# Performance work log

Hardware: AMD Instinct MI355X
Metric: run time of the kernel (lower is better)

Reference implementation:

```python
import jax, jax.numpy as jnp
import numpy as np

B, T, N, DIN, H, E, K, HM, CH, HOR, DOUT = 64, 12, 307, 1, 64, 10, 2, 16, 14, 12, 1
EPS = 1e-12


def setup_inputs() -> dict:
    key = jax.random.key(0)
    ks = jax.random.split(key, 16)
    rn = lambda k, s, sc=0.1: jax.random.normal(k, s, dtype=jnp.float32) * sc
    return {
        "hyper_source": jax.random.normal(ks[0], (B, CH, T, N), dtype=jnp.float32),
        "source": jax.random.normal(ks[1], (B, T, N, DIN), dtype=jnp.float32),
        "adj": jax.random.uniform(ks[2], (N, N), dtype=jnp.float32),
        "node_embeddings": rn(ks[3], (N, E), 1.0),
        "main_weights_pool": rn(ks[4], (E, H, DIN)),
        "hyper_W": rn(ks[5], (CH, H)),
        "hyper_b": jnp.zeros((H,), jnp.float32),
        "mask_W1": rn(ks[6], (H, HM)),
        "mask_W2": rn(ks[7], (HM, E)),
        "gate_Wpool": rn(ks[8], (E, K, 2 * DIN + H, 2 * H)),
        "gate_bpool": rn(ks[9], (E, 2 * H)),
        "upd_Wpool": rn(ks[10], (E, K, 2 * DIN + H, H)),
        "upd_bpool": rn(ks[11], (E, H)),
        "ln_gamma": jnp.ones((H,), jnp.float32),
        "ln_beta": jnp.zeros((H,), jnp.float32),
        "end_W": rn(ks[12], (HOR * DOUT, H)),
        "end_b": jnp.zeros((HOR * DOUT,), jnp.float32),
    }


def _forward(hyper_source, source, adj, node_embeddings, main_weights_pool,
             hyper_W, hyper_b, mask_W1, mask_W2, gate_Wpool, gate_bpool,
             upd_Wpool, upd_bpool, ln_gamma, ln_beta, end_W, end_b):
    # HyperNet: chunked long-history signal -> per-node per-step hidden h [B,N,T,H]
    h = jnp.tanh(jnp.einsum('bctn,ch->bnth', hyper_source, hyper_W) + hyper_b)
    # adaptive input channel: einsum('bnld,ndi->blni') with per-node weights
    weights_h = jnp.einsum('nd,dhi->nhi', node_embeddings, main_weights_pool)  # [N,H,DIN]
    x_adapt = jnp.einsum('bnlh,nhi->blni', h, weights_h)                       # [B,T,N,DIN]
    x = jnp.concatenate([x_adapt, source], axis=-1)                            # [B,T,N,2*DIN]
    # static Chebyshev supports (cheb_k=2): identity + mix(normalized adj, adaptive graph)
    adj_n = adj / jnp.clip(adj.sum(-1, keepdims=True), 1e-6)
    adapt = jax.nn.softmax(jax.nn.relu(node_embeddings @ node_embeddings.T), axis=1)
    A = 0.5 * (adj_n + adapt)
    supports = jnp.stack([jnp.eye(N, dtype=x.dtype), A])                       # [K,N,N]
    # per-node graph-conv weights generated from node embeddings
    gate_W = jnp.einsum('nd,dkio->nkio', node_embeddings, gate_Wpool)
    gate_b = node_embeddings @ gate_bpool
    upd_W = jnp.einsum('nd,dkio->nkio', node_embeddings, upd_Wpool)
    upd_b = node_embeddings @ upd_bpool

    def gconv(sup_b, xin, Wn, bn):
        xg = jnp.einsum('bknm,bmi->bnki', sup_b, xin)
        return jnp.einsum('bnki,nkio->bno', xg, Wn) + bn

    def step(state, inp):
        xt, ht = inp  # [B,N,2*DIN], [B,N,H]
        # dynamic graph sparsification mask from hypernet state
        logits = jnp.einsum('bne,me->bnm', (ht @ mask_W1) @ mask_W2, node_embeddings)
        mask = jax.nn.sigmoid(logits)                # [B,N,N]
        sup_b = supports[None] * mask[:, None]       # [B,K,N,N]
        xs = jnp.concatenate([xt, state], axis=-1)
        zr = jax.nn.sigmoid(gconv(sup_b, xs, gate_W, gate_b))
        z, r = jnp.split(zr, 2, axis=-1)
        cand = jnp.concatenate([xt, z * state], axis=-1)
        hc = jnp.tanh(gconv(sup_b, cand, upd_W, upd_b))
        return r * state + (1.0 - r) * hc, None

    init = jnp.zeros((x.shape[0], N, H), x.dtype)
    state, _ = jax.lax.scan(step, init,
                            (jnp.swapaxes(x, 0, 1), jnp.transpose(h, (2, 0, 1, 3))))
    # layernorm(eps=1e-12); dropout is identity at eval
    mu = state.mean(-1, keepdims=True)
    var = ((state - mu) ** 2).mean(-1, keepdims=True)
    xn = (state - mu) / jnp.sqrt(var + EPS) * ln_gamma + ln_beta
    # end_conv: Conv2d(1, HOR*DOUT, kernel=(1,H)) == per-node linear H -> HOR*DOUT
    out = jnp.einsum('bnh,oh->bon', xn, end_W) + end_b[None, :, None]
    out = out.reshape(-1, HOR, DOUT, N).transpose(0, 1, 3, 2)  # [B,HOR,N,DOUT]
    return out


def reference(hyper_source, source, adj, node_embeddings, main_weights_pool,
              hyper_W, hyper_b, mask_W1, mask_W2, gate_Wpool, gate_bpool,
              upd_Wpool, upd_bpool, ln_gamma, ln_beta, end_W, end_b):
    return _forward(hyper_source, source, adj, node_embeddings, main_weights_pool,
                    hyper_W, hyper_b, mask_W1, mask_W2, gate_Wpool, gate_bpool,
                    upd_Wpool, upd_bpool, ln_gamma, ln_beta, end_W, end_b)
```

## Files before the change

### kernel.cpp

```cpp
#include <hip/hip_runtime.h>
#include <hip/hip_bf16.h>

#define N_ 307
#define B_ 64
#define T_ 12
#define H_ 64
#define E_ 10
#define CH_ 14
#define HM_ 16
#define I2_ 66
#define GO_ 128
#define UO_ 64
#define QG_ (2 * I2_ * GO_)
#define QU_ (2 * I2_ * UO_)
#define TBN_ (T_ * B_ * N_)
#define WMP_ 320

__device__ __forceinline__ float wsum(float v) {
    #pragma unroll
    for (int off = 32; off; off >>= 1) v += __shfl_xor(v, off);
    return v;
}
__device__ __forceinline__ float wmax(float v) {
    #pragma unroll
    for (int off = 32; off; off >>= 1) v = fmaxf(v, __shfl_xor(v, off));
    return v;
}
__device__ __forceinline__ float sigm(float x) { return 1.f / (1.f + __expf(-x)); }
__device__ __forceinline__ float ftanh(float x) { return 1.f - 2.f / (__expf(2.f * x) + 1.f); }
__device__ __forceinline__ float bcast(float v, int l) {
    return __int_as_float(__builtin_amdgcn_readlane(__float_as_int(v), l));
}
__device__ __forceinline__ unsigned short f2bf(float f) {
    unsigned u = __float_as_uint(f);
    u += 0x7FFFu + ((u >> 16) & 1u);
    return (unsigned short)(u >> 16);
}
__device__ __forceinline__ float bf2f(unsigned short s) {
    return __uint_as_float((unsigned)s << 16);
}

__global__ void A_kernel(const float* __restrict__ adj, const float* __restrict__ nemb,
                         float* __restrict__ A) {
    const int n = blockIdx.x;
    const int lane = threadIdx.x;
    float en[E_];
    #pragma unroll
    for (int d = 0; d < E_; ++d) en[d] = nemb[n * E_ + d];
    float asum = 0.f;
    for (int m = lane; m < N_; m += 64) asum += adj[n * N_ + m];
    asum = fmaxf(wsum(asum), 1e-6f);
    float g[5]; bool valid[5];
    float mx = -1e30f;
    #pragma unroll
    for (int it = 0; it < 5; ++it) {
        int m = lane + it * 64;
        valid[it] = (m < N_);
        float dt = 0.f;
        if (valid[it]) {
            #pragma unroll
            for (int e = 0; e < E_; ++e) dt += en[e] * nemb[m * E_ + e];
            dt = fmaxf(dt, 0.f);
            mx = fmaxf(mx, dt);
        }
        g[it] = dt;
    }
    mx = wmax(mx);
    float se = 0.f;
    #pragma unroll
    for (int it = 0; it < 5; ++it)
        if (valid[it]) { g[it] = __expf(g[it] - mx); se += g[it]; }
    se = wsum(se);
    float inv = 1.f / se;
    #pragma unroll
    for (int it = 0; it < 5; ++it) {
        int m = lane + it * 64;
        if (valid[it]) A[n * N_ + m] = 0.5f * (adj[n * N_ + m] / asum + g[it] * inv);
    }
}

__device__ __forceinline__ float embdot(const float* __restrict__ nemb, int n,
                                        const float* __restrict__ pool, int Q, int q) {
    float a = 0.f;
    #pragma unroll
    for (int d = 0; d < E_; ++d) a += nemb[n * E_ + d] * pool[d * Q + q];
    return a;
}

__global__ __launch_bounds__(256) void gen_kernel(
    const float* __restrict__ nemb,
    const float* __restrict__ gWp, const float* __restrict__ gbp,
    const float* __restrict__ uWp, const float* __restrict__ ubp,
    const float* __restrict__ mwp,
    const float* __restrict__ W1, const float* __restrict__ W2,
    float* __restrict__ gW, float* __restrict__ gb,
    float* __restrict__ uW, float* __restrict__ ub,
    float* __restrict__ wh_t, float* __restrict__ W12) {
    const int e0 = N_ * QG_;
    const int e1 = e0 + N_ * GO_;
    const int e2 = e1 + N_ * QU_;
    const int e3 = e2 + N_ * UO_;
    const int e4 = e3 + N_ * H_;
    const int e5 = e4 + H_ * E_;
    int idx = blockIdx.x * 256 + threadIdx.x;
    if (idx < e0) {
        int n = idx / QG_, q = idx % QG_;
        gW[idx] = embdot(nemb, n, gWp, QG_, q);
    } else if (idx < e1) {
        int i = idx - e0; int n = i / GO_, q = i % GO_;
        gb[i] = embdot(nemb, n, gbp, GO_, q);
    } else if (idx < e2) {
        int i = idx - e1; int n = i / QU_, q = i % QU_;
        uW[i] = embdot(nemb, n, uWp, QU_, q);
    } else if (idx < e3) {
        int i = idx - e2; int n = i / UO_, q = i % UO_;
        ub[i] = embdot(nemb, n, ubp, UO_, q);
    } else if (idx < e4) {
        int i = idx - e3; int n = i / H_, q = i % H_;
        wh_t[q * N_ + n] = embdot(nemb, n, mwp, H_, q);
    } else if (idx < e5) {
        int i = idx - e4; int j = i / E_, e = i % E_;
        float a = 0.f;
        #pragma unroll
        for (int q = 0; q < HM_; ++q) a += W1[j * HM_ + q] * W2[q * E_ + e];
        W12[i] = a;
    }
}

__global__ __launch_bounds__(256) void hyper2_kernel(
    const float* __restrict__ hs, const float* __restrict__ src,
    const float* __restrict__ hyper_W, const float* __restrict__ hyper_b,
    const float* __restrict__ wh_t, const float* __restrict__ W12,
    float* __restrict__ x0, float* __restrict__ x1, float* __restrict__ emb) {
    const int tb = blockIdx.y;
    const int t = tb / B_, b = tb % B_;
    const int n = blockIdx.x * 256 + threadIdx.x;
    const bool act = (n < N_);
    const int nc = act ? n : N_ - 1;
    float hsv[CH_];
    #pragma unroll
    for (int c = 0; c < CH_; ++c)
        hsv[c] = hs[((b * CH_ + c) * T_ + t) * N_ + nc];
    float ax0 = 0.f;
    float ae[E_] = {};
    #pragma unroll 8
    for (int j = 0; j < H_; ++j) {
        float hj = hyper_b[j];
        #pragma unroll
        for (int c = 0; c < CH_; ++c) hj = fmaf(hsv[c], hyper_W[c * H_ + j], hj);
        hj = ftanh(hj);
        ax0 = fmaf(hj, wh_t[j * N_ + nc], ax0);
        #pragma unroll
        for (int e = 0; e < E_; ++e) ae[e] = fmaf(hj, W12[j * E_ + e], ae[e]);
    }
    if (act) {
        const int tbn = tb * N_ + n;
        x0[tbn] = ax0;
        x1[tbn] = src[(b * T_ + t) * N_ + n];
        #pragma unroll
        for (int e = 0; e < E_; ++e) emb[e * TBN_ + tbn] = ae[e];
    }
}

__global__ __launch_bounds__(256) void wm_kernel(
    const float* __restrict__ A, const float* __restrict__ emb,
    const float* __restrict__ nemb, const float* __restrict__ x0,
    const float* __restrict__ x1, unsigned short* __restrict__ Wm,
    float* __restrict__ dmask, float* __restrict__ aggx, int t) {
    const int wid = __builtin_amdgcn_readfirstlane(blockIdx.x * 4 + (threadIdx.x >> 6));
    const int lane = threadIdx.x & 63;
    const int b = wid / N_;
    const int n = wid % N_;
    const int tbn = (t * B_ + b) * N_ + n;
    const int xb = tbn - n;
    float et[E_];
    #pragma unroll
    for (int d = 0; d < E_; ++d) et[d] = emb[(size_t)d * TBN_ + tbn];
    unsigned short* wr = Wm + (size_t)(b * N_ + n) * WMP_;
    float a0 = 0.f, a1 = 0.f;
    #pragma unroll
    for (int c = 0; c < 5; ++c) {
        int m = c * 64 + lane;
        bool v = (m < N_);
        int mc = v ? m : 0;
        float dt = 0.f;
        #pragma unroll
        for (int d = 0; d < E_; ++d) dt += et[d] * nemb[mc * E_ + d];
        float sg = sigm(dt);
        float w = v ? A[n * N_ + mc] * sg : 0.f;
        wr[m] = v ? f2bf(w) : (unsigned short)0;
        if (v) {
            if (m == n) dmask[tbn] = sg;
            a0 += w * x0[xb + mc];
            a1 += w * x1[xb + mc];
        }
    }
    a0 = wsum(a0);
    a1 = wsum(a1);
    if (lane == 0) {
        aggx[(size_t)tbn * 2] = a0;
        aggx[(size_t)tbn * 2 + 1] = a1;
    }
}

__global__ __launch_bounds__(512) void aggS_kernel(
    const unsigned short* __restrict__ Wm, const float* __restrict__ Sin,
    float* __restrict__ aggS) {
    __shared__ float s_lds[128 * 64];
    const int tid = threadIdx.x;
    const int lane = tid & 63;
    const int wv = tid >> 6;
    const int b = blockIdx.y;
    const int nb = blockIdx.x * 32 + wv * 4;
    int roff[4];
    #pragma unroll
    for (int r = 0; r < 4; ++r) {
        int nr = nb + r; if (nr > N_ - 1) nr = N_ - 1;
        roff[r] = __builtin_amdgcn_readfirstlane((b * N_ + nr) * WMP_);
    }
    float acc[4] = {0.f, 0.f, 0.f, 0.f};
    const float4* s4 = (const float4*)(Sin + (size_t)b * N_ * 64);
    float4* d4 = (float4*)s_lds;
    #pragma unroll
    for (int sck = 0; sck < 3; ++sck) {
        const int mbase = sck * 128;
        const int nrows = (sck < 2) ? 128 : 64;
        if (sck) __syncthreads();
        for (int idx = tid; idx < nrows * 16; idx += 512) {
            int row = mbase + (idx >> 4);
            int rc = (row < N_) ? row : N_ - 1;
            d4[idx] = s4[rc * 16 + (idx & 15)];
        }
        __syncthreads();
        for (int sub = 0; sub < nrows; sub += 64) {
            const int m0 = mbase + sub;
            float wf0 = bf2f(Wm[roff[0] + m0 + lane]);
            float wf1 = bf2f(Wm[roff[1] + m0 + lane]);
            float wf2 = bf2f(Wm[roff[2] + m0 + lane]);
            float wf3 = bf2f(Wm[roff[3] + m0 + lane]);
            #pragma unroll 8
            for (int mm = 0; mm < 64; ++mm) {
                float sv = s_lds[(sub + mm) * 64 + lane];
                acc[0] = fmaf(bcast(wf0, mm), sv, acc[0]);
                acc[1] = fmaf(bcast(wf1, mm), sv, acc[1]);
                acc[2] = fmaf(bcast(wf2, mm), sv, acc[2]);
                acc[3] = fmaf(bcast(wf3, mm), sv, acc[3]);
            }
        }
    }
    #pragma unroll
    for (int r = 0; r < 4; ++r) {
        int nr = nb + r;
        if (nr < N_) aggS[((size_t)b * N_ + nr) * 64 + lane] = acc[r];
    }
}

__global__ __launch_bounds__(256) void gate_mm_kernel(
    const float* __restrict__ gate_W, const float* __restrict__ gate_b,
    const float* __restrict__ x0, const float* __restrict__ x1,
    const float* __restrict__ S, const float* __restrict__ dmask,
    const float* __restrict__ aggx, const float* __restrict__ aggS,
    float* __restrict__ zs, float* __restrict__ rbuf, int t) {
    __shared__ float W_s[132][64];
    __shared__ float xg_s[64][132];
    const int oh = blockIdx.x, n = blockIdx.y;
    const int tid = threadIdx.x;
    for (int idx = tid; idx < 132 * 64; idx += 256) {
        int row = idx >> 6, op = idx & 63;
        int col = (op < 32) ? (oh * 32 + op) : (64 + oh * 32 + (op - 32));
        W_s[row][op] = gate_W[(n * 132 + row) * GO_ + col];
    }
    for (int idx = tid; idx < 64 * 132; idx += 256) {
        int b = idx / 132, i = idx % 132;
        int tb = (t * B_ + b) * N_ + n;
        float v;
        if (i < 66) {
            float xs = (i == 0) ? x0[tb] : (i == 1) ? x1[tb] : S[(b * N_ + n) * 64 + (i - 2)];
            v = dmask[tb] * xs;
        } else {
            int i2 = i - 66;
            v = (i2 < 2) ? aggx[(size_t)tb * 2 + i2] : aggS[(b * N_ + n) * 64 + (i2 - 2)];
        }
        xg_s[b][i] = v;
    }
    __syncthreads();
    const int bl = (tid >> 3) * 2, og = tid & 7;
    float acc[2][8] = {};
    for (int i = 0; i < 132; ++i) {
        float xv0 = xg_s[bl][i], xv1 = xg_s[bl + 1][i];
        #pragma unroll
        for (int r = 0; r < 8; ++r) {
            float wv = W_s[i][og * 8 + r];
            acc[0][r] = fmaf(xv0, wv, acc[0][r]);
            acc[1][r] = fmaf(xv1, wv, acc[1][r]);
        }
    }
    __syncthreads();
    float* zr_s = &xg_s[0][0];
    #pragma unroll
    for (int q = 0; q < 2; ++q) {
        #pragma unroll
        for (int r = 0; r < 8; ++r) {
            int op = og * 8 + r;
            int col = (op < 32) ? (oh * 32 + op) : (64 + oh * 32 + (op - 32));
            zr_s[(bl + q) * 64 + op] = sigm(acc[q][r] + gate_b[n * GO_ + col]);
        }
    }
    __syncthreads();
    for (int idx = tid; idx < 64 * 32; idx += 256) {
        int b = idx >> 5, jl = idx & 31;
        int j = oh * 32 + jl;
        float z = zr_s[b * 64 + jl];
        float rr = zr_s[b * 64 + 32 + jl];
        int sidx = (b * N_ + n) * 64 + j;
        zs[sidx] = z * S[sidx];
        rbuf[sidx] = rr;
    }
}

__global__ __launch_bounds__(256) void upd_mm_kernel(
    const float* __restrict__ upd_W, const float* __restrict__ upd_b,
    const float* __restrict__ x0, const float* __restrict__ x1,
    const float* __restrict__ zsrc, const float* __restrict__ dmask,
    const float* __restrict__ aggx, const float* __restrict__ aggS,
    const float* __restrict__ rbuf, float* __restrict__ S, int t) {
    __shared__ float W_s[132][64];
    __shared__ float xg_s[64][132];
    const int n = blockIdx.x;
    const int tid = threadIdx.x;
    for (int idx = tid; idx < 132 * 64; idx += 256) {
        int row = idx >> 6, op = idx & 63;
        W_s[row][op] = upd_W[(n * 132 + row) * UO_ + op];
    }
    for (int idx = tid; idx < 64 * 132; idx += 256) {
        int b = idx / 132, i = idx % 132;
        int tb = (t * B_ + b) * N_ + n;
        float v;
        if (i < 66) {
            float xs = (i == 0) ? x0[tb] : (i == 1) ? x1[tb] : zsrc[(b * N_ + n) * 64 + (i - 2)];
            v = dmask[tb] * xs;
        } else {
            int i2 = i - 66;
            v = (i2 < 2) ? aggx[(size_t)tb * 2 + i2] : aggS[(b * N_ + n) * 64 + (i2 - 2)];
        }
        xg_s[b][i] = v;
    }
    __syncthreads();
    const int bl = (tid >> 3) * 2, og = tid & 7;
    float acc[2][8] = {};
    for (int i = 0; i < 132; ++i) {
        float xv0 = xg_s[bl][i], xv1 = xg_s[bl + 1][i];
        #pragma unroll
        for (int r = 0; r < 8; ++r) {
            float wv = W_s[i][og * 8 + r];
            acc[0][r] = fmaf(xv0, wv, acc[0][r]);
            acc[1][r] = fmaf(xv1, wv, acc[1][r]);
        }
    }
    #pragma unroll
    for (int q = 0; q < 2; ++q) {
        int b = bl + q;
        #pragma unroll
        for (int r = 0; r < 8; ++r) {
            int op = og * 8 + r;
            float hc = ftanh(acc[q][r] + upd_b[n * UO_ + op]);
            int sidx = (b * N_ + n) * 64 + op;
            float rr = rbuf[sidx];
            float sv = S[sidx];
            S[sidx] = rr * sv + (1.f - rr) * hc;
        }
    }
}

__global__ __launch_bounds__(256) void final_kernel(
    const float* __restrict__ S, const float* __restrict__ gamma,
    const float* __restrict__ beta, const float* __restrict__ endW,
    const float* __restrict__ endb, float* __restrict__ out) {
    const int wid = blockIdx.x * 4 + (threadIdx.x >> 6);
    const int lane = threadIdx.x & 63;
    const int b = wid / N_, n = wid % N_;
    float s = S[wid * 64 + lane];
    float mu = wsum(s) * (1.f / 64.f);
    float d = s - mu;
    float var = wsum(d * d) * (1.f / 64.f);
    float xn = d / sqrtf(var + 1e-12f) * gamma[lane] + beta[lane];
    #pragma unroll
    for (int o = 0; o < 12; ++o) {
        float dot = wsum(xn * endW[o * 64 + lane]);
        if (lane == o) out[(b * 12 + o) * N_ + n] = dot + endb[o];
    }
}

extern "C" void kernel_launch(void* const* d_in, const int* in_sizes, int n_in,
                              void* d_out, int out_size, void* d_ws, size_t ws_size,
                              hipStream_t stream) {
    const float* hyper_source = (const float*)d_in[0];
    const float* source       = (const float*)d_in[1];
    const float* adj          = (const float*)d_in[2];
    const float* nemb         = (const float*)d_in[3];
    const float* mwpool       = (const float*)d_in[4];
    const float* hyper_W      = (const float*)d_in[5];
    const float* hyper_b      = (const float*)d_in[6];
    const float* mask_W1      = (const float*)d_in[7];
    const float* mask_W2      = (const float*)d_in[8];
    const float* gate_Wpool   = (const float*)d_in[9];
    const float* gate_bpool   = (const float*)d_in[10];
    const float* upd_Wpool    = (const float*)d_in[11];
    const float* upd_bpool    = (const float*)d_in[12];
    const float* ln_gamma     = (const float*)d_in[13];
    const float* ln_beta      = (const float*)d_in[14];
    const float* end_W        = (const float*)d_in[15];
    const float* end_b        = (const float*)d_in[16];
    float* out = (float*)d_out;

    float* ws = (float*)d_ws;
    size_t off = 0;
    auto alloc = [&](size_t nf) {
        float* p = ws + off;
        off += (nf + 255) & ~(size_t)255;
        return p;
    };
    float* A      = alloc((size_t)N_ * N_);
    float* wh_t   = alloc((size_t)N_ * H_);
    float* W12    = alloc((size_t)H_ * E_);
    float* gate_W = alloc((size_t)N_ * QG_);
    float* gate_b = alloc((size_t)N_ * GO_);
    float* upd_W  = alloc((size_t)N_ * QU_);
    float* upd_b  = alloc((size_t)N_ * UO_);
    float* x0     = alloc((size_t)TBN_);
    float* x1     = alloc((size_t)TBN_);
    float* emb    = alloc((size_t)TBN_ * E_);
    float* dmask  = alloc((size_t)TBN_);
    float* aggx   = alloc((size_t)TBN_ * 2);
    float* S      = alloc((size_t)B_ * N_ * H_);
    float* zs     = alloc((size_t)B_ * N_ * H_);
    float* rbuf   = alloc((size_t)B_ * N_ * H_);
    float* aggS   = alloc((size_t)B_ * N_ * H_);
    unsigned short* Wm = (unsigned short*)alloc((size_t)B_ * N_ * WMP_ / 2);

    hipMemsetAsync(S, 0, (size_t)B_ * N_ * H_ * sizeof(float), stream);

    A_kernel<<<N_, 64, 0, stream>>>(adj, nemb, A);

    const int gen_total = N_ * QG_ + N_ * GO_ + N_ * QU_ + N_ * UO_ + N_ * H_ + H_ * E_;
    gen_kernel<<<(gen_total + 255) / 256, 256, 0, stream>>>(
        nemb, gate_Wpool, gate_bpool, upd_Wpool, upd_bpool, mwpool, mask_W1, mask_W2,
        gate_W, gate_b, upd_W, upd_b, wh_t, W12);

    hyper2_kernel<<<dim3(2, T_ * B_), 256, 0, stream>>>(hyper_source, source, hyper_W,
                                                        hyper_b, wh_t, W12, x0, x1, emb);

    for (int t = 0; t < T_; ++t) {
        wm_kernel<<<(B_ * N_) / 4, 256, 0, stream>>>(A, emb, nemb, x0, x1, Wm, dmask, aggx, t);
        aggS_kernel<<<dim3(10, B_), 512, 0, stream>>>(Wm, S, aggS);
        gate_mm_kernel<<<dim3(2, N_), 256, 0, stream>>>(gate_W, gate_b, x0, x1, S, dmask,
                                                        aggx, aggS, zs, rbuf, t);
        aggS_kernel<<<dim3(10, B_), 512, 0, stream>>>(Wm, zs, aggS);
        upd_mm_kernel<<<N_, 256, 0, stream>>>(upd_W, upd_b, x0, x1, zs, dmask, aggx,
                                              aggS, rbuf, S, t);
    }

    final_kernel<<<(B_ * N_) / 4, 256, 0, stream>>>(S, ln_gamma, ln_beta, end_W, end_b, out);
}
```

Before: 2.623 ms.

## Retile gate and update GEMMs with register blocking and direct global weight reads

Both per-node gate and update kernels stop staging weights in shared memory. Each thread now reads its weight row slice directly from global memory as float4 or float2, and computes a 4x4 or 4x2 register tile against a transposed, padded input tile. The gate kernel now assigns the z half to one block and the r half to the other, which removes a shared-memory round trip and extra barriers. The update kernel now launches two blocks per node, doubling parallelism. The costs are float4 LDS reads at an odd row stride (67), which may be misaligned, and weight reads that depend on cache hits.

```diff
diff --git a/kernel.cpp b/kernel.cpp
--- a/kernel.cpp
+++ b/kernel.cpp
@@ -15,6 +15,7 @@
 #define QU_ (2 * I2_ * UO_)
 #define TBN_ (T_ * B_ * N_)
 #define WMP_ 320
+#define XLD_ 67
 
 __device__ __forceinline__ float wsum(float v) {
     #pragma unroll
@@ -261,15 +262,9 @@
     const float* __restrict__ S, const float* __restrict__ dmask,
     const float* __restrict__ aggx, const float* __restrict__ aggS,
     float* __restrict__ zs, float* __restrict__ rbuf, int t) {
-    __shared__ float W_s[132][64];
-    __shared__ float xg_s[64][132];
+    __shared__ float xgT[132 * XLD_];
     const int oh = blockIdx.x, n = blockIdx.y;
     const int tid = threadIdx.x;
-    for (int idx = tid; idx < 132 * 64; idx += 256) {
-        int row = idx >> 6, op = idx & 63;
-        int col = (op < 32) ? (oh * 32 + op) : (64 + oh * 32 + (op - 32));
-        W_s[row][op] = gate_W[(n * 132 + row) * GO_ + col];
-    }
     for (int idx = tid; idx < 64 * 132; idx += 256) {
         int b = idx / 132, i = idx % 132;
         int tb = (t * B_ + b) * N_ + n;
@@ -281,40 +276,35 @@
             int i2 = i - 66;
             v = (i2 < 2) ? aggx[(size_t)tb * 2 + i2] : aggS[(b * N_ + n) * 64 + (i2 - 2)];
         }
-        xg_s[b][i] = v;
+        xgT[i * XLD_ + b] = v;
     }
     __syncthreads();
-    const int bl = (tid >> 3) * 2, og = tid & 7;
-    float acc[2][8] = {};
+    const int b0 = (tid & 15) * 4;
+    const int c0 = (tid >> 4) * 4;
+    const float* wp = gate_W + (size_t)n * 132 * GO_ + oh * 64 + c0;
+    float acc[4][4] = {};
     for (int i = 0; i < 132; ++i) {
-        float xv0 = xg_s[bl][i], xv1 = xg_s[bl + 1][i];
-        #pragma unroll
-        for (int r = 0; r < 8; ++r) {
-            float wv = W_s[i][og * 8 + r];
-            acc[0][r] = fmaf(xv0, wv, acc[0][r]);
-            acc[1][r] = fmaf(xv1, wv, acc[1][r]);
-        }
-    }
-    __syncthreads();
-    float* zr_s = &xg_s[0][0];
-    #pragma unroll
-    for (int q = 0; q < 2; ++q) {
-        #pragma unroll
-        for (int r = 0; r < 8; ++r) {
-            int op = og * 8 + r;
-            int col = (op < 32) ? (oh * 32 + op) : (64 + oh * 32 + (op - 32));
-            zr_s[(bl + q) * 64 + op] = sigm(acc[q][r] + gate_b[n * GO_ + col]);
-        }
-    }
-    __syncthreads();
-    for (int idx = tid; idx < 64 * 32; idx += 256) {
-        int b = idx >> 5, jl = idx & 31;
-        int j = oh * 32 + jl;
-        float z = zr_s[b * 64 + jl];
-        float rr = zr_s[b * 64 + 32 + jl];
-        int sidx = (b * N_ + n) * 64 + j;
-        zs[sidx] = z * S[sidx];
-        rbuf[sidx] = rr;
+        float4 xv = *(const float4*)&xgT[i * XLD_ + b0];
+        float4 wv = *(const float4*)&wp[(size_t)i * GO_];
+        float xa[4] = {xv.x, xv.y, xv.z, xv.w};
+        float wa[4] = {wv.x, wv.y, wv.z, wv.w};
+        #pragma unroll
+        for (int bq = 0; bq < 4; ++bq)
+            #pragma unroll
+            for (int cq = 0; cq < 4; ++cq)
+                acc[bq][cq] = fmaf(xa[bq], wa[cq], acc[bq][cq]);
+    }
+    const float* gb = gate_b + n * GO_ + oh * 64 + c0;
+    float bias[4] = {gb[0], gb[1], gb[2], gb[3]};
+    #pragma unroll
+    for (int bq = 0; bq < 4; ++bq) {
+        const int sbase = ((b0 + bq) * N_ + n) * 64 + c0;
+        #pragma unroll
+        for (int cq = 0; cq < 4; ++cq) {
+            float g = sigm(acc[bq][cq] + bias[cq]);
+            if (oh == 0) zs[sbase + cq] = g * S[sbase + cq];
+            else         rbuf[sbase + cq] = g;
+        }
     }
 }
 
@@ -324,14 +314,9 @@
     const float* __restrict__ zsrc, const float* __restrict__ dmask,
     const float* __restrict__ aggx, const float* __restrict__ aggS,
     const float* __restrict__ rbuf, float* __restrict__ S, int t) {
-    __shared__ float W_s[132][64];
-    __shared__ float xg_s[64][132];
-    const int n = blockIdx.x;
+    __shared__ float xgT[132 * XLD_];
+    const int oh = blockIdx.x, n = blockIdx.y;
     const int tid = threadIdx.x;
-    for (int idx = tid; idx < 132 * 64; idx += 256) {
-        int row = idx >> 6, op = idx & 63;
-        W_s[row][op] = upd_W[(n * 132 + row) * UO_ + op];
-    }
     for (int idx = tid; idx < 64 * 132; idx += 256) {
         int b = idx / 132, i = idx % 132;
         int tb = (t * B_ + b) * N_ + n;
@@ -343,31 +328,34 @@
             int i2 = i - 66;
             v = (i2 < 2) ? aggx[(size_t)tb * 2 + i2] : aggS[(b * N_ + n) * 64 + (i2 - 2)];
         }
-        xg_s[b][i] = v;
+        xgT[i * XLD_ + b] = v;
     }
     __syncthreads();
-    const int bl = (tid >> 3) * 2, og = tid & 7;
-    float acc[2][8] = {};
+    const int b0 = (tid & 15) * 4;
+    const int c0 = (tid >> 4) * 2 + oh * 32;
+    const float* wp = upd_W + (size_t)n * 132 * UO_ + c0;
+    float acc[4][2] = {};
     for (int i = 0; i < 132; ++i) {
-        float xv0 = xg_s[bl][i], xv1 = xg_s[bl + 1][i];
-        #pragma unroll
-        for (int r = 0; r < 8; ++r) {
-            float wv = W_s[i][og * 8 + r];
-            acc[0][r] = fmaf(xv0, wv, acc[0][r]);
-            acc[1][r] = fmaf(xv1, wv, acc[1][r]);
-        }
-    }
-    #pragma unroll
-    for (int q = 0; q < 2; ++q) {
-        int b = bl + q;
-        #pragma unroll
-        for (int r = 0; r < 8; ++r) {
-            int op = og * 8 + r;
-            float hc = ftanh(acc[q][r] + upd_b[n * UO_ + op]);
-            int sidx = (b * N_ + n) * 64 + op;
-            float rr = rbuf[sidx];
-            float sv = S[sidx];
-            S[sidx] = rr * sv + (1.f - rr) * hc;
+        float4 xv = *(const float4*)&xgT[i * XLD_ + b0];
+        float2 wv = *(const float2*)&wp[(size_t)i * UO_];
+        float xa[4] = {xv.x, xv.y, xv.z, xv.w};
+        #pragma unroll
+        for (int bq = 0; bq < 4; ++bq) {
+            acc[bq][0] = fmaf(xa[bq], wv.x, acc[bq][0]);
+            acc[bq][1] = fmaf(xa[bq], wv.y, acc[bq][1]);
+        }
+    }
+    const float bias0 = upd_b[n * UO_ + c0];
+    const float bias1 = upd_b[n * UO_ + c0 + 1];
+    #pragma unroll
+    for (int bq = 0; bq < 4; ++bq) {
+        const int sbase = ((b0 + bq) * N_ + n) * 64 + c0;
+        #pragma unroll
+        for (int cq = 0; cq < 2; ++cq) {
+            float hc = ftanh(acc[bq][cq] + (cq ? bias1 : bias0));
+            float rr = rbuf[sbase + cq];
+            float sv = S[sbase + cq];
+            S[sbase + cq] = rr * sv + (1.f - rr) * hc;
         }
     }
 }
@@ -456,8 +444,8 @@
         gate_mm_kernel<<<dim3(2, N_), 256, 0, stream>>>(gate_W, gate_b, x0, x1, S, dmask,
                                                         aggx, aggS, zs, rbuf, t);
         aggS_kernel<<<dim3(10, B_), 512, 0, stream>>>(Wm, zs, aggS);
-        upd_mm_kernel<<<N_, 256, 0, stream>>>(upd_W, upd_b, x0, x1, zs, dmask, aggx,
-                                              aggS, rbuf, S, t);
+        upd_mm_kernel<<<dim3(2, N_), 256, 0, stream>>>(upd_W, upd_b, x0, x1, zs, dmask, aggx,
+                                                       aggS, rbuf, S, t);
     }
 
     final_kernel<<<(B_ * N_) / 4, 256, 0, stream>>>(S, ln_gamma, ln_beta, end_W, end_b, out);
```

Result: faster. 2.460 ms (-6.2%).
